# Optimization experiments

Hardware: AMD Instinct MI355X
Metric: run time of the kernel (lower is better)

## Reference

```python
import jax, jax.numpy as jnp
import numpy as np

T_STEPS = 100
T_EMB = 16
EPS = 1e-8


def sin_emb(t, dim):
    # sinusoidal_time_embedding: [cos(t*f), sin(t*f)] with f = exp(-log(1e4)*i/half)
    half = dim // 2
    freqs = jnp.exp(-jnp.log(jnp.float32(10000.0)) * jnp.arange(half, dtype=jnp.float32) / half)
    a = t.astype(jnp.float32)[:, None] * freqs[None, :]
    return jnp.concatenate([jnp.cos(a), jnp.sin(a)], axis=-1)


def lstm_layer(x_tbf, W_ih, W_hh, b):
    # x_tbf: [T, B, F]; torch gate order i, f, g, o
    B = x_tbf.shape[1]
    H = W_hh.shape[1]

    def step(carry, x_t):
        h, c = carry
        g = x_t @ W_ih.T + h @ W_hh.T + b
        i, f, gg, o = jnp.split(g, 4, axis=-1)
        c = jax.nn.sigmoid(f) * c + jax.nn.sigmoid(i) * jnp.tanh(gg)
        h = jax.nn.sigmoid(o) * jnp.tanh(c)
        return (h, c), h

    z = jnp.zeros((B, H), x_tbf.dtype)
    (h, c), ys = jax.lax.scan(step, (z, z), x_tbf)
    return ys, h


def _forward(x_hist, x_future, y0, turb_idx, pred_steps, init_noise, turb_emb,
             W_ih0, W_hh0, b_ih0, b_hh0, W_ih1, W_hh1, b_ih1, b_hh1,
             W1, b1, W2, b2, W3, b3):
    betas = jnp.linspace(1e-4, 0.02, T_STEPS).astype(jnp.float32)
    alphas = 1.0 - betas
    alpha_bars = jnp.cumprod(alphas)

    B = x_hist.shape[0]
    emb = turb_emb[turb_idx]  # [B, E]
    eh = jnp.broadcast_to(emb[:, None, :], (B, x_hist.shape[1], emb.shape[1]))
    ef = jnp.broadcast_to(emb[:, None, :], (B, x_future.shape[1], emb.shape[1]))
    xh = jnp.concatenate([x_hist, eh], axis=-1).transpose(1, 0, 2)    # [T_in, B, F+E]
    xf = jnp.concatenate([x_future, ef], axis=-1).transpose(1, 0, 2)  # [P, B, exo+E]

    ys0, _ = lstm_layer(xh, W_ih0, W_hh0, b_ih0 + b_hh0)
    _, enc_out = lstm_layer(ys0, W_ih1, W_hh1, b_ih1 + b_hh1)         # [B, H] = h[-1]

    def mlp(x):
        h = jax.nn.relu(x @ W1.T + b1)
        h = jax.nn.relu(h @ W2.T + b2)
        return h @ W3.T + b3

    def ar_step(prev_y, xs):
        exo_t, step, y_init = xs
        cond = jnp.concatenate([enc_out, exo_t, prev_y], axis=1)  # [B, cond_dim]
        h_e = sin_emb(jnp.full((B,), step), T_EMB)

        def dstep(y, t):
            t_e = sin_emb(jnp.full((B,), t), T_EMB)
            eps_hat = mlp(jnp.concatenate([cond, y, t_e, h_e], axis=1))  # [B,1]
            b_t, a_t, ab_t = betas[t], alphas[t], alpha_bars[t]
            pred_x0 = (y - jnp.sqrt(1.0 - ab_t) * eps_hat) / (jnp.sqrt(ab_t) + EPS)
            mean = (y - b_t / (jnp.sqrt(1.0 - ab_t) + EPS) * eps_hat) / (jnp.sqrt(a_t) + EPS)
            # eval mode -> deterministic sampling: posterior noise term is zero
            return jnp.where(t == 0, pred_x0, mean), None

        y, _ = jax.lax.scan(dstep, y_init, jnp.arange(T_STEPS - 1, -1, -1))
        return y, y[:, 0]

    _, seq = jax.lax.scan(ar_step, y0, (xf, jnp.arange(pred_steps), init_noise))
    return seq.T[:, :, None]  # [B, pred_steps, 1]


def setup_inputs() -> dict:
    key = jax.random.key(0)
    ks = list(jax.random.split(key, 24))
    kit = iter(ks)
    B, T_IN, F_IN, EXO, EMB, PRED, HID, NTURB = 1024, 96, 8, 6, 16, 8, 128, 100
    in0 = F_IN + EMB                 # 24
    cond_dim = HID + EXO + EMB + 1   # 151
    in_mlp = cond_dim + 1 + T_EMB + T_EMB  # 184

    def nrm(shape, s=0.05):
        return jax.random.normal(next(kit), shape, jnp.float32) * s

    return {
        'x_hist': jax.random.normal(next(kit), (B, T_IN, F_IN), jnp.float32),
        'x_future': jax.random.normal(next(kit), (B, PRED, EXO), jnp.float32),
        'y0': jnp.zeros((B, 1), jnp.float32),
        'turb_idx': jax.random.randint(next(kit), (B,), 0, NTURB),
        'pred_steps': PRED,
        'init_noise': jax.random.normal(next(kit), (PRED, B, 1), jnp.float32),
        'turb_emb': nrm((NTURB, EMB), 0.1),
        'W_ih0': nrm((4 * HID, in0)), 'W_hh0': nrm((4 * HID, HID)),
        'b_ih0': jnp.zeros((4 * HID,), jnp.float32), 'b_hh0': jnp.zeros((4 * HID,), jnp.float32),
        'W_ih1': nrm((4 * HID, HID)), 'W_hh1': nrm((4 * HID, HID)),
        'b_ih1': jnp.zeros((4 * HID,), jnp.float32), 'b_hh1': jnp.zeros((4 * HID,), jnp.float32),
        'W1': nrm((HID, in_mlp)), 'b1': jnp.zeros((HID,), jnp.float32),
        'W2': nrm((HID, HID)), 'b2': jnp.zeros((HID,), jnp.float32),
        'W3': nrm((1, HID)), 'b3': jnp.zeros((1,), jnp.float32),
    }


def reference(x_hist, x_future, y0, turb_idx, pred_steps, init_noise, turb_emb,
              W_ih0, W_hh0, b_ih0, b_hh0, W_ih1, W_hh1, b_ih1, b_hh1,
              W1, b1, W2, b2, W3, b3):
    return _forward(x_hist, x_future, y0, turb_idx, pred_steps, init_noise, turb_emb,
                    W_ih0, W_hh0, b_ih0, b_hh0, W_ih1, W_hh1, b_ih1, b_hh1,
                    W1, b1, W2, b2, W3, b3)
```

## Files before the change

kernel.cpp:

```cpp
#include <hip/hip_runtime.h>
#include <hip/hip_fp16.h>
#include <stdint.h>


typedef __attribute__((ext_vector_type(2))) _Float16 half2_t;
typedef __attribute__((ext_vector_type(8))) _Float16 v8h;
typedef __attribute__((ext_vector_type(4))) float v4f;

#define DEV __device__ __forceinline__

DEV uint32_t pack2f(float a, float b) {
  __half ha = __float2half_rn(a), hb = __float2half_rn(b);
  return (uint32_t)__half_as_ushort(ha) | ((uint32_t)__half_as_ushort(hb) << 16);
}

DEV float2 up2(uint32_t u) {
  half2_t h = __builtin_bit_cast(half2_t, u);
  return make_float2((float)h.x, (float)h.y);
}

DEV float fast_ex2(float x) {
#if __has_builtin(__builtin_amdgcn_exp2f)
  return __builtin_amdgcn_exp2f(x);
#else
  return exp2f(x);
#endif
}
DEV float fast_rcp(float x) {
#if __has_builtin(__builtin_amdgcn_rcpf)
  return __builtin_amdgcn_rcpf(x);
#else
  return 1.f / x;
#endif
}
DEV float sigm(float x) { return fast_rcp(1.f + fast_ex2(-1.4426950408889634f * x)); }
DEV float tanh_f(float x) {
  return 2.f * fast_rcp(1.f + fast_ex2(-2.8853900817779268f * x)) - 1.f;
}

DEV uint32_t pk_h1(uint32_t b, uint32_t t, uint32_t wy, uint32_t yP) {
  half2_t hb = __builtin_bit_cast(half2_t, b);
  half2_t ht = __builtin_bit_cast(half2_t, t);
  half2_t hw = __builtin_bit_cast(half2_t, wy);
  half2_t hy = __builtin_bit_cast(half2_t, yP);
  half2_t r = hb + ht + hw * hy;
  half2_t z = {(_Float16)0.f, (_Float16)0.f};
#if __has_builtin(__builtin_elementwise_max)
  r = __builtin_elementwise_max(r, z);
#else
  uint32_t u = __builtin_bit_cast(uint32_t, r);
  uint32_t mask = ((u >> 15) & 1u) * 0xFFFFu | ((u >> 31) & 1u) * 0xFFFF0000u;
  r = __builtin_bit_cast(half2_t, u & ~mask);
#endif
  return __builtin_bit_cast(uint32_t, r);
}

DEV float rowsum16(float v) {
  int x;
  x = __builtin_amdgcn_update_dpp(0, __builtin_bit_cast(int, v), 0x111, 0xf, 0xf, true);
  v += __builtin_bit_cast(float, x);
  x = __builtin_amdgcn_update_dpp(0, __builtin_bit_cast(int, v), 0x112, 0xf, 0xf, true);
  v += __builtin_bit_cast(float, x);
  x = __builtin_amdgcn_update_dpp(0, __builtin_bit_cast(int, v), 0x114, 0xf, 0xf, true);
  v += __builtin_bit_cast(float, x);
  x = __builtin_amdgcn_update_dpp(0, __builtin_bit_cast(int, v), 0x118, 0xf, 0xf, true);
  v += __builtin_bit_cast(float, x);
  return v;
}

static constexpr size_t OFF_XH  = 0;
static constexpr size_t OFF_W0  = 4718592;
static constexpr size_t OFF_BS0 = 4882432;
static constexpr size_t OFF_W1L = 4884480;
static constexpr size_t OFF_BS1 = 5146624;
static constexpr size_t OFF_W2P = 5148672;
static constexpr size_t OFF_ENC = 5181440;
static constexpr size_t OFF_YS0 = 5705728;

__global__ void k_prep_xh(const float* __restrict__ xh, const int* __restrict__ tix,
                          const float* __restrict__ temb, uint32_t* __restrict__ out) {
  int idx = blockIdx.x * 256 + threadIdx.x;
  if (idx >= 96 * 1024 * 12) return;
  int m = idx % 12;
  int tb = idx / 12;
  int b = tb & 1023, t = tb >> 10;
  int k0 = 2 * m, k1 = k0 + 1;
  float v0 = (k0 < 8) ? xh[(b * 96 + t) * 8 + k0] : temb[tix[b] * 16 + (k0 - 8)];
  float v1 = (k1 < 8) ? xh[(b * 96 + t) * 8 + k1] : temb[tix[b] * 16 + (k1 - 8)];
  out[idx] = pack2f(v0, v1);
}

__global__ void k_prep_w(const float* __restrict__ Wih0, const float* __restrict__ Whh0,
                         const float* __restrict__ bih0, const float* __restrict__ bhh0,
                         const float* __restrict__ Wih1, const float* __restrict__ Whh1,
                         const float* __restrict__ bih1, const float* __restrict__ bhh1,
                         const float* __restrict__ W2,
                         uint32_t* __restrict__ w0p, uint32_t* __restrict__ w1p,
                         uint32_t* __restrict__ w2p, float* __restrict__ bs0,
                         float* __restrict__ bs1) {
  int idx = blockIdx.x * 256 + threadIdx.x;
  if (idx < 40960) {
    int w = idx / 5120;
    int r = idx % 5120;
    int T = r / 1280; r %= 1280;
    int f = r / 256;  r %= 256;
    int l = r >> 2, c = r & 3;
    int m = l & 15, qf = l >> 4;
    int g = (m & 3) * 128 + w * 16 + (m >> 2) * 4 + T;
    int k0 = f * 32 + qf * 8 + 2 * c, k1 = k0 + 1;
    float a = (k0 < 24) ? Wih0[g * 24 + k0] : ((k0 < 152) ? Whh0[g * 128 + k0 - 24] : 0.f);
// ... 61 lines not shown
    uint32_t sx = 0;
    int sb = 0, sm = 0;
    if (t < 95 && tid < 192) {
      sb = tid / 12; sm = tid % 12;
      sx = xh16[((t + 1) * 1024 + bbase + sb) * 12 + sm];
    }
    v4f acc[4];
#pragma unroll
    for (int T = 0; T < 4; T++) acc[T] = (v4f){0.f, 0.f, 0.f, 0.f};
#pragma unroll
    for (int f = 0; f < 5; f++) {
      uint4 bu = *(const uint4*)&inb[cur][n][f * 32 + ql * 8];
      v8h Bv = __builtin_bit_cast(v8h, bu);
#pragma unroll
      for (int T = 0; T < 4; T++)
        acc[T] = __builtin_amdgcn_mfma_f32_16x16x32_f16(
            __builtin_bit_cast(v8h, Af[T][f]), Bv, acc[T], 0, 0, 0);
    }
    float hv[4];
#pragma unroll
    for (int T = 0; T < 4; T++) {
      float gi = acc[T][0] + bias[T][0];
      float gf = acc[T][1] + bias[T][1];
      float gg = acc[T][2] + bias[T][2];
      float go = acc[T][3] + bias[T][3];
      float c = sigm(gf) * cst[T] + sigm(gi) * tanh_f(gg);
      cst[T] = c;
      hv[T] = sigm(go) * tanh_f(c);
    }
    uint32_t h01 = pack2f(hv[0], hv[1]), h23 = pack2f(hv[2], hv[3]);
    *(uint2*)&inb[nxt][n][24 + ju] = make_uint2(h01, h23);
    *(uint2*)((__half*)ys0 + (size_t)(t * 1024 + bbase + n) * 128 + ju) = make_uint2(h01, h23);
    if (t < 95 && tid < 192) ((uint32_t*)&inb[nxt][sb][0])[sm] = sx;
    __syncthreads();
  }
}

__global__ __launch_bounds__(512, 2) void k_lstm1(const uint32_t* __restrict__ ys0u,
                                                  const uint32_t* __restrict__ w1A,
                                                  const float* __restrict__ bs1,
                                                  float* __restrict__ enc) {
  __shared__ __align__(16) __half inb[2][16][264];
  const int tid = threadIdx.x;
  const int w = tid >> 6, l = tid & 63;
  const int n = l & 15, ql = l >> 4;
  const int ju = w * 16 + ql * 4;
  const int bbase = blockIdx.x * 16;
  const int sb = tid >> 5, sc = tid & 31;

  uint4 Af[4][8];
#pragma unroll
  for (int T = 0; T < 4; T++)
#pragma unroll
    for (int f = 0; f < 8; f++)
      Af[T][f] = ((const uint4*)w1A)[((w * 4 + T) * 8 + f) * 64 + l];
  float bias[4][4];
#pragma unroll
  for (int T = 0; T < 4; T++)
#pragma unroll
    for (int r = 0; r < 4; r++) bias[T][r] = bs1[r * 128 + ju + T];

  for (int i = tid; i < 4224; i += 512) ((uint32_t*)inb)[i] = 0u;
  __syncthreads();
  {
    uint2 v = ((const uint2*)ys0u)[(size_t)(0 * 1024 + bbase + sb) * 32 + sc];
    *(uint2*)&inb[0][sb][sc * 4] = v;
  }
// ... 2 lines not shown

  for (int t = 0; t < 96; t++) {
    const int cur = t & 1, nxt = cur ^ 1;
    uint2 sv = make_uint2(0u, 0u);
    if (t < 95)
      sv = ((const uint2*)ys0u)[(size_t)((t + 1) * 1024 + bbase + sb) * 32 + sc];
    v4f acc[4];
#pragma unroll
    for (int T = 0; T < 4; T++) acc[T] = (v4f){0.f, 0.f, 0.f, 0.f};
#pragma unroll
    for (int f = 0; f < 8; f++) {
      uint4 bu = *(const uint4*)&inb[cur][n][f * 32 + ql * 8];
      v8h Bv = __builtin_bit_cast(v8h, bu);
#pragma unroll
      for (int T = 0; T < 4; T++)
        acc[T] = __builtin_amdgcn_mfma_f32_16x16x32_f16(
            __builtin_bit_cast(v8h, Af[T][f]), Bv, acc[T], 0, 0, 0);
    }
    float hv[4];
#pragma unroll
    for (int T = 0; T < 4; T++) {
      float gi = acc[T][0] + bias[T][0];
      float gf = acc[T][1] + bias[T][1];
      float gg = acc[T][2] + bias[T][2];
      float go = acc[T][3] + bias[T][3];
      float c = sigm(gf) * cst[T] + sigm(gi) * tanh_f(gg);
      cst[T] = c;
      hv[T] = sigm(go) * tanh_f(c);
    }
    *(uint2*)&inb[nxt][n][128 + ju] = make_uint2(pack2f(hv[0], hv[1]), pack2f(hv[2], hv[3]));
    if (t < 95) *(uint2*)&inb[nxt][sb][sc * 4] = sv;
    if (t == 95)
      *(float4*)&enc[(size_t)(bbase + n) * 128 + ju] = make_float4(hv[0], hv[1], hv[2], hv[3]);
    __syncthreads();
  }
}

__global__ __launch_bounds__(256, 1) void k_diff(
    const float* __restrict__ xfut, const float* __restrict__ y0,
    const int* __restrict__ tix, const float* __restrict__ noise,
    const float* __restrict__ temb, const float* __restrict__ W1,
    const float* __restrict__ b1, const float* __restrict__ b2,
    const float* __restrict__ W3, const float* __restrict__ b3,
    const uint32_t* __restrict__ w2p, const float* __restrict__ enc,
    float* __restrict__ out) {
  __shared__ __align__(16) uint32_t W1sL[128 * 64];
  __shared__ __align__(16) uint32_t W1xL[128 * 28];
  __shared__ __align__(16) uint32_t encPL[16 * 64];
  __shared__ uint32_t embPL[16 * 8];
  __shared__ float teL[100][16];
  __shared__ float2 ccL[100];
  __shared__ __align__(16) __half tprojL[100 * 128];
  __shared__ __half hprojL[8 * 128];
  __shared__ __align__(16) float partL[2][4][16];
  __shared__ uint32_t encdL[256 * 17];

  const int tid = threadIdx.x;
  const int w = tid >> 6, l = tid & 63;
  const int m = l & 15, q = l >> 4;
  const int bbase = blockIdx.x * 16;

  for (int i = tid; i < 128 * 64; i += 256) {
    int r = i >> 6, c = i & 63;
    W1sL[i] = pack2f(W1[r * 184 + 2 * c], W1[r * 184 + 2 * c + 1]);
  }
  for (int i = tid; i < 128 * 28; i += 256) {
    int r = i / 28, c = i % 28;
    W1xL[i] = pack2f(W1[r * 184 + 128 + 2 * c], W1[r * 184 + 129 + 2 * c]);
  }
  for (int i = tid; i < 16 * 64; i += 256) {
    int bb = i >> 6, c = i & 63;
    encPL[i] = pack2f(enc[(bbase + bb) * 128 + 2 * c], enc[(bbase + bb) * 128 + 2 * c + 1]);
  }
  for (int i = tid; i < 16 * 8; i += 256) {
    int bb = i >> 3, c = i & 7;
    const float* er = temb + tix[bbase + bb] * 16;
    embPL[i] = pack2f(er[2 * c], er[2 * c + 1]);
  }
  for (int p = tid; p < 1600; p += 256) {
    int tt = p >> 4, i = p & 15;
    float f = expf(-logf(10000.f) * (float)(i & 7) / 8.f);
    float a = (float)tt * f;
    teL[tt][i] = (i < 8) ? cosf(a) : sinf(a);
  }
  for (int qq = tid; qq < 100; qq += 256) {
    float ab = 1.f, beta = 0.f;
    for (int i = 0; i <= qq; i++) {
      beta = 1e-4f + (0.02f - 1e-4f) * (float)i / 99.f;
      ab *= (1.f - beta);
    }
    float cs, cd;
    if (qq == 0) { cs = sqrtf(1.f - ab); cd = 1.f / (sqrtf(ab) + 1e-8f); }
    else { cs = beta / (sqrtf(1.f - ab) + 1e-8f); cd = 1.f / (sqrtf(1.f - beta) + 1e-8f); }
    ccL[qq] = make_float2(cs, cd);
  }
  __syncthreads();

  {
    int k = tid & 127, hs = tid >> 7;
    float wte[16], whe[16];
#pragma unroll
    for (int i = 0; i < 8; i++) {
      float2 a = up2(W1xL[k * 28 + 12 + i]);
      wte[2 * i] = a.x; wte[2 * i + 1] = a.y;
      float2 bqq = up2(W1xL[k * 28 + 20 + i]);
      whe[2 * i] = bqq.x; whe[2 * i + 1] = bqq.y;
    }
    for (int tt = hs * 50; tt < hs * 50 + 50; tt++) {
      float s = 0.f;
#pragma unroll
      for (int i = 0; i < 16; i++) s += wte[i] * teL[tt][i];
      tprojL[tt * 128 + k] = __float2half_rn(s);
    }
    if (hs == 0) {
      for (int ss = 0; ss < 8; ss++) {
        float s = 0.f;
#pragma unroll
        for (int i = 0; i < 16; i++) s += whe[i] * teL[ss][i];
        hprojL[ss * 128 + k] = __float2half_rn(s);
      }
    }
  }

  for (int pi = 0; pi < 16; pi++) {
    int k0 = (pi >> 2) * 32 + q * 8 + (pi & 3) * 2;
    half2_t a0 = {(_Float16)0.f, (_Float16)0.f};
    half2_t a1 = a0;
    const uint32_t* wr0 = &W1sL[k0 * 64];
    const uint32_t* wr1 = &W1sL[(k0 + 1) * 64];
    const uint32_t* ep = &encPL[m * 64];
#pragma unroll 8
    for (int c = 0; c < 64; c++) {
      half2_t e = __builtin_bit_cast(half2_t, ep[c]);
      a0 += __builtin_bit_cast(half2_t, wr0[c]) * e;
      a1 += __builtin_bit_cast(half2_t, wr1[c]) * e;
    }
#pragma unroll
    for (int c = 0; c < 8; c++) {
      half2_t e = __builtin_bit_cast(half2_t, embPL[m * 8 + c]);
      a0 += __builtin_bit_cast(half2_t, W1xL[k0 * 28 + 3 + c]) * e;
      a1 += __builtin_bit_cast(half2_t, W1xL[(k0 + 1) * 28 + 3 + c]) * e;
    }
    float e0 = b1[k0] + (float)a0.x + (float)a0.y;
    float e1 = b1[k0 + 1] + (float)a1.x + (float)a1.y;
    encdL[tid * 17 + pi] = pack2f(e0, e1);
  }

  uint4 Bf[2][4];
  const uint4* w2u4 = (const uint4*)w2p;
#pragma unroll
  for (int tt = 0; tt < 2; tt++) {
    int n = w * 32 + tt * 16 + m;
#pragma unroll
    for (int f = 0; f < 4; f++) Bf[tt][f] = w2u4[n * 16 + f * 4 + q];
  }
  const float w3v0 = W3[w * 32 + m], w3v1 = W3[w * 32 + 16 + m];
  const float b2v0 = b2[w * 32 + m], b2v1 = b2[w * 32 + 16 + m];
  const float b3v = b3[0];

  uint32_t w1yP[16];
#pragma unroll
  for (int pi = 0; pi < 16; pi++) {
    int k0 = (pi >> 2) * 32 + q * 8 + (pi & 3) * 2;
    uint32_t ua = W1xL[k0 * 28 + 11];
    uint32_t ub = W1xL[(k0 + 1) * 28 + 11];
    w1yP[pi] = (ua >> 16) | (ub & 0xFFFF0000u);
  }

  float prev_y = y0[bbase + m];
  __syncthreads();

  int buf = 0;
  for (int s = 0; s < 8; s++) {
    float xf[6];
#pragma unroll
    for (int i = 0; i < 6; i++) xf[i] = xfut[((bbase + m) * 8 + s) * 6 + i];
    uint32_t bph[16];
#pragma unroll
    for (int pi = 0; pi < 16; pi++) {
      int k0 = (pi >> 2) * 32 + q * 8 + (pi & 3) * 2;
      float2 ed = up2(encdL[tid * 17 + pi]);
      float e0 = ed.x, e1 = ed.y;
#pragma unroll
      for (int c = 0; c < 3; c++) {
        float2 w0v = up2(W1xL[k0 * 28 + c]);
        float2 w1v = up2(W1xL[(k0 + 1) * 28 + c]);
        e0 += w0v.x * xf[2 * c] + w0v.y * xf[2 * c + 1];
        e1 += w1v.x * xf[2 * c] + w1v.y * xf[2 * c + 1];
      }
      e0 += up2(W1xL[k0 * 28 + 11]).x * prev_y;
      e1 += up2(W1xL[(k0 + 1) * 28 + 11]).x * prev_y;
      e0 += (float)hprojL[s * 128 + k0];
      e1 += (float)hprojL[s * 128 + k0 + 1];
      bph[pi] = pack2f(e0, e1);
    }

    float y = noise[s * 1024 + bbase + m];
    for (int t = 99; t >= 0; t--) {
      const uint4* tp = (const uint4*)(tprojL + t * 128 + q * 8);
      uint32_t yP = pack2f(y, y);
      v4f c0 = {0.f, 0.f, 0.f, 0.f}, c1 = c0;
#pragma unroll
      for (int f = 0; f < 4; f++) {
        uint4 tv = tp[f * 4];
        uint4 au;
        au.x = pk_h1(bph[f * 4 + 0], tv.x, w1yP[f * 4 + 0], yP);
        au.y = pk_h1(bph[f * 4 + 1], tv.y, w1yP[f * 4 + 1], yP);
        au.z = pk_h1(bph[f * 4 + 2], tv.z, w1yP[f * 4 + 2], yP);
        au.w = pk_h1(bph[f * 4 + 3], tv.w, w1yP[f * 4 + 3], yP);
        v8h A = __builtin_bit_cast(v8h, au);
        c0 = __builtin_amdgcn_mfma_f32_16x16x32_f16(A, __builtin_bit_cast(v8h, Bf[0][f]), c0, 0, 0, 0);
        c1 = __builtin_amdgcn_mfma_f32_16x16x32_f16(A, __builtin_bit_cast(v8h, Bf[1][f]), c1, 0, 0, 0);
      }
      float pr[4];
#pragma unroll
      for (int r = 0; r < 4; r++) {
        pr[r] = fmaxf(c0[r] + b2v0, 0.f) * w3v0 + fmaxf(c1[r] + b2v1, 0.f) * w3v1;
        pr[r] = rowsum16(pr[r]);
      }
      if ((l & 15) == 15)
        *(float4*)&partL[buf][w][q * 4] = make_float4(pr[0], pr[1], pr[2], pr[3]);
      __syncthreads();
      float2 cc = ccL[t];
      float eps = b3v + partL[buf][0][m] + partL[buf][1][m] +
                  partL[buf][2][m] + partL[buf][3][m];
      y = (y - cc.x * eps) * cc.y;
      buf ^= 1;
    }
    if (w == 0 && l < 16) out[(bbase + l) * 8 + s] = y;
    prev_y = y;
  }
}

extern "C" void kernel_launch(void* const* d_in, const int* in_sizes, int n_in,
                              void* d_out, int out_size, void* d_ws, size_t ws_size,
                              hipStream_t stream) {
  const float* x_hist    = (const float*)d_in[0];
  const float* x_future  = (const float*)d_in[1];
  const float* y0        = (const float*)d_in[2];
  const int*   turb_idx  = (const int*)d_in[3];
  const float* init_noise = (const float*)d_in[5];
  const float* turb_emb  = (const float*)d_in[6];
  const float* W_ih0     = (const float*)d_in[7];
  const float* W_hh0     = (const float*)d_in[8];
  const float* b_ih0     = (const float*)d_in[9];
  const float* b_hh0     = (const float*)d_in[10];
  const float* W_ih1     = (const float*)d_in[11];
  const float* W_hh1     = (const float*)d_in[12];
  const float* b_ih1     = (const float*)d_in[13];
  const float* b_hh1     = (const float*)d_in[14];
  const float* W1        = (const float*)d_in[15];
  const float* b1        = (const float*)d_in[16];
  const float* W2        = (const float*)d_in[17];
  const float* b2        = (const float*)d_in[18];
  const float* W3        = (const float*)d_in[19];
  const float* b3        = (const float*)d_in[20];

  char* ws = (char*)d_ws;
  uint32_t* xh16 = (uint32_t*)(ws + OFF_XH);
  uint32_t* w0p  = (uint32_t*)(ws + OFF_W0);
  float*    bs0  = (float*)(ws + OFF_BS0);
  uint32_t* w1p  = (uint32_t*)(ws + OFF_W1L);
  float*    bs1  = (float*)(ws + OFF_BS1);
  uint32_t* w2p  = (uint32_t*)(ws + OFF_W2P);
  float*    encf = (float*)(ws + OFF_ENC);
  __half*   ys0h = (__half*)(ws + OFF_YS0);

  k_prep_xh<<<4608, 256, 0, stream>>>(x_hist, turb_idx, turb_emb, xh16);
  k_prep_w<<<452, 256, 0, stream>>>(W_ih0, W_hh0, b_ih0, b_hh0,
                                    W_ih1, W_hh1, b_ih1, b_hh1,
                                    W2, w0p, w1p, w2p, bs0, bs1);
  k_lstm0<<<64, 512, 0, stream>>>(xh16, w0p, bs0, ys0h);
  k_lstm1<<<64, 512, 0, stream>>>((const uint32_t*)ys0h, w1p, bs1, encf);
  k_diff<<<64, 256, 0, stream>>>(x_future, y0, turb_idx, init_noise, turb_emb,
                                 W1, b1, b2, W3, b3, w2p, encf, (float*)d_out);
}
```

Before: 724.9 us.

## Prefetch next-step time projection and shorten the serial diffusion step chain

Inside the 100-step denoising loop, the next timestep's time projection and coefficients are loaded and pre-added to the bias before the barrier, so only a packed FMA plus ReLU sits on the y-dependent path. The MFMA accumulation is split into two independent chains to reduce dependency stalls, y is converted with a packed round-toward-zero convert, and noise is loaded once up front. Shared-memory weight arrays are padded to odd strides to avoid bank conflicts in the setup GEMV. This raises register pressure, and the rounding mode of the y conversion changes slightly.

```diff
diff --git a/kernel.cpp b/kernel.cpp
--- a/kernel.cpp
+++ b/kernel.cpp
@@ -38,12 +38,14 @@
   return 2.f * fast_rcp(1.f + fast_ex2(-2.8853900817779268f * x)) - 1.f;
 }
 
-DEV uint32_t pk_h1(uint32_t b, uint32_t t, uint32_t wy, uint32_t yP) {
-  half2_t hb = __builtin_bit_cast(half2_t, b);
-  half2_t ht = __builtin_bit_cast(half2_t, t);
-  half2_t hw = __builtin_bit_cast(half2_t, wy);
-  half2_t hy = __builtin_bit_cast(half2_t, yP);
-  half2_t r = hb + ht + hw * hy;
+DEV uint32_t pk_add(uint32_t a, uint32_t b) {
+  return __builtin_bit_cast(uint32_t,
+      __builtin_bit_cast(half2_t, a) + __builtin_bit_cast(half2_t, b));
+}
+
+DEV uint32_t pk_relufma(uint32_t w, uint32_t y, uint32_t b) {
+  half2_t r = __builtin_bit_cast(half2_t, w) * __builtin_bit_cast(half2_t, y) +
+              __builtin_bit_cast(half2_t, b);
   half2_t z = {(_Float16)0.f, (_Float16)0.f};
 #if __has_builtin(__builtin_elementwise_max)
   r = __builtin_elementwise_max(r, z);
@@ -53,6 +55,14 @@
   r = __builtin_bit_cast(half2_t, u & ~mask);
 #endif
   return __builtin_bit_cast(uint32_t, r);
+}
+
+DEV uint32_t cvtpk(float y) {
+#if __has_builtin(__builtin_amdgcn_cvt_pkrtz)
+  return __builtin_bit_cast(uint32_t, __builtin_amdgcn_cvt_pkrtz(y, y));
+#else
+  return pack2f(y, y);
+#endif
 }
 
 DEV float rowsum16(float v) {
@@ -284,10 +294,10 @@
     const float* __restrict__ W3, const float* __restrict__ b3,
     const uint32_t* __restrict__ w2p, const float* __restrict__ enc,
     float* __restrict__ out) {
-  __shared__ __align__(16) uint32_t W1sL[128 * 64];
-  __shared__ __align__(16) uint32_t W1xL[128 * 28];
-  __shared__ __align__(16) uint32_t encPL[16 * 64];
-  __shared__ uint32_t embPL[16 * 8];
+  __shared__ uint32_t W1sL[128 * 65];
+  __shared__ uint32_t W1xL[128 * 29];
+  __shared__ uint32_t encPL[16 * 65];
+  __shared__ uint32_t embPL[16 * 9];
   __shared__ float teL[100][16];
   __shared__ float2 ccL[100];
   __shared__ __align__(16) __half tprojL[100 * 128];
@@ -302,20 +312,21 @@
 
   for (int i = tid; i < 128 * 64; i += 256) {
     int r = i >> 6, c = i & 63;
-    W1sL[i] = pack2f(W1[r * 184 + 2 * c], W1[r * 184 + 2 * c + 1]);
+    W1sL[r * 65 + c] = pack2f(W1[r * 184 + 2 * c], W1[r * 184 + 2 * c + 1]);
   }
   for (int i = tid; i < 128 * 28; i += 256) {
     int r = i / 28, c = i % 28;
-    W1xL[i] = pack2f(W1[r * 184 + 128 + 2 * c], W1[r * 184 + 129 + 2 * c]);
+    W1xL[r * 29 + c] = pack2f(W1[r * 184 + 128 + 2 * c], W1[r * 184 + 129 + 2 * c]);
   }
   for (int i = tid; i < 16 * 64; i += 256) {
     int bb = i >> 6, c = i & 63;
-    encPL[i] = pack2f(enc[(bbase + bb) * 128 + 2 * c], enc[(bbase + bb) * 128 + 2 * c + 1]);
+    encPL[bb * 65 + c] = pack2f(enc[(bbase + bb) * 128 + 2 * c],
+                                enc[(bbase + bb) * 128 + 2 * c + 1]);
   }
   for (int i = tid; i < 16 * 8; i += 256) {
     int bb = i >> 3, c = i & 7;
     const float* er = temb + tix[bbase + bb] * 16;
-    embPL[i] = pack2f(er[2 * c], er[2 * c + 1]);
+    embPL[bb * 9 + c] = pack2f(er[2 * c], er[2 * c + 1]);
   }
   for (int p = tid; p < 1600; p += 256) {
     int tt = p >> 4, i = p & 15;
@@ -341,9 +352,9 @@
     float wte[16], whe[16];
 #pragma unroll
     for (int i = 0; i < 8; i++) {
-      float2 a = up2(W1xL[k * 28 + 12 + i]);
+      float2 a = up2(W1xL[k * 29 + 12 + i]);
       wte[2 * i] = a.x; wte[2 * i + 1] = a.y;
-      float2 bqq = up2(W1xL[k * 28 + 20 + i]);
+      float2 bqq = up2(W1xL[k * 29 + 20 + i]);
       whe[2 * i] = bqq.x; whe[2 * i + 1] = bqq.y;
     }
     for (int tt = hs * 50; tt < hs * 50 + 50; tt++) {
@@ -366,9 +377,9 @@
     int k0 = (pi >> 2) * 32 + q * 8 + (pi & 3) * 2;
     half2_t a0 = {(_Float16)0.f, (_Float16)0.f};
     half2_t a1 = a0;
-    const uint32_t* wr0 = &W1sL[k0 * 64];
-    const uint32_t* wr1 = &W1sL[(k0 + 1) * 64];
-    const uint32_t* ep = &encPL[m * 64];
+    const uint32_t* wr0 = &W1sL[k0 * 65];
+    const uint32_t* wr1 = &W1sL[(k0 + 1) * 65];
+    const uint32_t* ep = &encPL[m * 65];
 #pragma unroll 8
     for (int c = 0; c < 64; c++) {
       half2_t e = __builtin_bit_cast(half2_t, ep[c]);
@@ -377,9 +388,9 @@
     }
 #pragma unroll
     for (int c = 0; c < 8; c++) {
-      half2_t e = __builtin_bit_cast(half2_t, embPL[m * 8 + c]);
-      a0 += __builtin_bit_cast(half2_t, W1xL[k0 * 28 + 3 + c]) * e;
-      a1 += __builtin_bit_cast(half2_t, W1xL[(k0 + 1) * 28 + 3 + c]) * e;
+      half2_t e = __builtin_bit_cast(half2_t, embPL[m * 9 + c]);
+      a0 += __builtin_bit_cast(half2_t, W1xL[k0 * 29 + 3 + c]) * e;
+      a1 += __builtin_bit_cast(half2_t, W1xL[(k0 + 1) * 29 + 3 + c]) * e;
     }
     float e0 = b1[k0] + (float)a0.x + (float)a0.y;
     float e1 = b1[k0 + 1] + (float)a1.x + (float)a1.y;
@@ -402,12 +413,15 @@
 #pragma unroll
   for (int pi = 0; pi < 16; pi++) {
     int k0 = (pi >> 2) * 32 + q * 8 + (pi & 3) * 2;
-    uint32_t ua = W1xL[k0 * 28 + 11];
-    uint32_t ub = W1xL[(k0 + 1) * 28 + 11];
+    uint32_t ua = W1xL[k0 * 29 + 11];
+    uint32_t ub = W1xL[(k0 + 1) * 29 + 11];
     w1yP[pi] = (ua >> 16) | (ub & 0xFFFF0000u);
   }
 
   float prev_y = y0[bbase + m];
+  float noi[8];
+#pragma unroll
+  for (int s = 0; s < 8; s++) noi[s] = noise[s * 1024 + bbase + m];
   __syncthreads();
 
   int buf = 0;
@@ -423,35 +437,58 @@
       float e0 = ed.x, e1 = ed.y;
 #pragma unroll
       for (int c = 0; c < 3; c++) {
-        float2 w0v = up2(W1xL[k0 * 28 + c]);
-        float2 w1v = up2(W1xL[(k0 + 1) * 28 + c]);
+        float2 w0v = up2(W1xL[k0 * 29 + c]);
+        float2 w1v = up2(W1xL[(k0 + 1) * 29 + c]);
         e0 += w0v.x * xf[2 * c] + w0v.y * xf[2 * c + 1];
         e1 += w1v.x * xf[2 * c] + w1v.y * xf[2 * c + 1];
       }
-      e0 += up2(W1xL[k0 * 28 + 11]).x * prev_y;
-      e1 += up2(W1xL[(k0 + 1) * 28 + 11]).x * prev_y;
+      e0 += up2(W1xL[k0 * 29 + 11]).x * prev_y;
+      e1 += up2(W1xL[(k0 + 1) * 29 + 11]).x * prev_y;
       e0 += (float)hprojL[s * 128 + k0];
       e1 += (float)hprojL[s * 128 + k0 + 1];
       bph[pi] = pack2f(e0, e1);
     }
 
-    float y = noise[s * 1024 + bbase + m];
+    float y = noi[s];
+    uint32_t bt[16];
+    {
+      const uint4* tb = (const uint4*)(tprojL + 99 * 128 + q * 8);
+      uint4 t0 = tb[0], t1 = tb[4], t2 = tb[8], t3 = tb[12];
+      bt[0] = pk_add(bph[0], t0.x);  bt[1] = pk_add(bph[1], t0.y);
+      bt[2] = pk_add(bph[2], t0.z);  bt[3] = pk_add(bph[3], t0.w);
+      bt[4] = pk_add(bph[4], t1.x);  bt[5] = pk_add(bph[5], t1.y);
+      bt[6] = pk_add(bph[6], t1.z);  bt[7] = pk_add(bph[7], t1.w);
+      bt[8] = pk_add(bph[8], t2.x);  bt[9] = pk_add(bph[9], t2.y);
+      bt[10] = pk_add(bph[10], t2.z); bt[11] = pk_add(bph[11], t2.w);
+      bt[12] = pk_add(bph[12], t3.x); bt[13] = pk_add(bph[13], t3.y);
+      bt[14] = pk_add(bph[14], t3.z); bt[15] = pk_add(bph[15], t3.w);
+    }
+    float2 ccv = ccL[99];
+
     for (int t = 99; t >= 0; t--) {
-      const uint4* tp = (const uint4*)(tprojL + t * 128 + q * 8);
-      uint32_t yP = pack2f(y, y);
-      v4f c0 = {0.f, 0.f, 0.f, 0.f}, c1 = c0;
+      uint32_t yP = cvtpk(y);
+      v4f c0a = {0.f, 0.f, 0.f, 0.f}, c0b = c0a, c1a = c0a, c1b = c0a;
 #pragma unroll
       for (int f = 0; f < 4; f++) {
-        uint4 tv = tp[f * 4];
         uint4 au;
-        au.x = pk_h1(bph[f * 4 + 0], tv.x, w1yP[f * 4 + 0], yP);
-        au.y = pk_h1(bph[f * 4 + 1], tv.y, w1yP[f * 4 + 1], yP);
-        au.z = pk_h1(bph[f * 4 + 2], tv.z, w1yP[f * 4 + 2], yP);
-        au.w = pk_h1(bph[f * 4 + 3], tv.w, w1yP[f * 4 + 3], yP);
+        au.x = pk_relufma(w1yP[4 * f + 0], yP, bt[4 * f + 0]);
+        au.y = pk_relufma(w1yP[4 * f + 1], yP, bt[4 * f + 1]);
+        au.z = pk_relufma(w1yP[4 * f + 2], yP, bt[4 * f + 2]);
+        au.w = pk_relufma(w1yP[4 * f + 3], yP, bt[4 * f + 3]);
         v8h A = __builtin_bit_cast(v8h, au);
-        c0 = __builtin_amdgcn_mfma_f32_16x16x32_f16(A, __builtin_bit_cast(v8h, Bf[0][f]), c0, 0, 0, 0);
-        c1 = __builtin_amdgcn_mfma_f32_16x16x32_f16(A, __builtin_bit_cast(v8h, Bf[1][f]), c1, 0, 0, 0);
+        if (f & 1) {
+          c0b = __builtin_amdgcn_mfma_f32_16x16x32_f16(A, __builtin_bit_cast(v8h, Bf[0][f]), c0b, 0, 0, 0);
+          c1b = __builtin_amdgcn_mfma_f32_16x16x32_f16(A, __builtin_bit_cast(v8h, Bf[1][f]), c1b, 0, 0, 0);
+        } else {
+          c0a = __builtin_amdgcn_mfma_f32_16x16x32_f16(A, __builtin_bit_cast(v8h, Bf[0][f]), c0a, 0, 0, 0);
+          c1a = __builtin_amdgcn_mfma_f32_16x16x32_f16(A, __builtin_bit_cast(v8h, Bf[1][f]), c1a, 0, 0, 0);
+        }
       }
+      const int tn = (t > 0) ? t - 1 : 0;
+      const uint4* tb = (const uint4*)(tprojL + tn * 128 + q * 8);
+      uint4 t0 = tb[0], t1 = tb[4], t2 = tb[8], t3 = tb[12];
+      float2 ccn = ccL[tn];
+      v4f c0 = c0a + c0b, c1 = c1a + c1b;
       float pr[4];
 #pragma unroll
       for (int r = 0; r < 4; r++) {
@@ -460,11 +497,22 @@
       }
       if ((l & 15) == 15)
         *(float4*)&partL[buf][w][q * 4] = make_float4(pr[0], pr[1], pr[2], pr[3]);
+      uint32_t btn[16];
+      btn[0] = pk_add(bph[0], t0.x);  btn[1] = pk_add(bph[1], t0.y);
+      btn[2] = pk_add(bph[2], t0.z);  btn[3] = pk_add(bph[3], t0.w);
+      btn[4] = pk_add(bph[4], t1.x);  btn[5] = pk_add(bph[5], t1.y);
+      btn[6] = pk_add(bph[6], t1.z);  btn[7] = pk_add(bph[7], t1.w);
+      btn[8] = pk_add(bph[8], t2.x);  btn[9] = pk_add(bph[9], t2.y);
+      btn[10] = pk_add(bph[10], t2.z); btn[11] = pk_add(bph[11], t2.w);
+      btn[12] = pk_add(bph[12], t3.x); btn[13] = pk_add(bph[13], t3.y);
+      btn[14] = pk_add(bph[14], t3.z); btn[15] = pk_add(bph[15], t3.w);
       __syncthreads();
-      float2 cc = ccL[t];
-      float eps = b3v + partL[buf][0][m] + partL[buf][1][m] +
-                  partL[buf][2][m] + partL[buf][3][m];
-      y = (y - cc.x * eps) * cc.y;
+      float eps = b3v + ((partL[buf][0][m] + partL[buf][1][m]) +
+                         (partL[buf][2][m] + partL[buf][3][m]));
+      y = (y - ccv.x * eps) * ccv.y;
+      ccv = ccn;
+#pragma unroll
+      for (int pi = 0; pi < 16; pi++) bt[pi] = btn[pi];
       buf ^= 1;
     }
     if (w == 0 && l < 16) out[(bbase + l) * 8 + s] = y;
```

Measured after the change: 675.7 us. 6.8% less time.

## Restructure diffusion sampler into single-wave blocks with precomputed conditioning

Applied to the files above, without the earlier changes.

Moves the per-sample conditioning projections (encoder, exogenous, embedding, step embedding), time-embedding projections and schedule coefficients into a new parallel prep kernel writing to workspace. The diffusion loop now runs one 64-lane wave per block handling 32 samples across all 128 hidden units, so the per-step cross-wave LDS reduction and __syncthreads are replaced by DPP row sums and shuffles. It also software-pipelines the next step's bias+tproj adds, and swaps the LSTM __syncthreads for a raw s_waitcnt+s_barrier. The trade-off is that only 32 blocks of one wave each are active, which lowers occupancy and puts the whole serial chain of 16 MFMAs per step on a single wave, while it adds an extra kernel launch and a workspace round trip.

```diff
diff --git a/kernel.cpp b/kernel.cpp
--- a/kernel.cpp
+++ b/kernel.cpp
@@ -9,14 +9,13 @@
 
 #define DEV __device__ __forceinline__
 
+DEV void barrier_lds() {
+  asm volatile("s_waitcnt lgkmcnt(0)\ns_barrier" ::: "memory");
+}
+
 DEV uint32_t pack2f(float a, float b) {
   __half ha = __float2half_rn(a), hb = __float2half_rn(b);
   return (uint32_t)__half_as_ushort(ha) | ((uint32_t)__half_as_ushort(hb) << 16);
-}
-
-DEV float2 up2(uint32_t u) {
-  half2_t h = __builtin_bit_cast(half2_t, u);
-  return make_float2((float)h.x, (float)h.y);
 }
 
 DEV float fast_ex2(float x) {
@@ -38,12 +37,20 @@
   return 2.f * fast_rcp(1.f + fast_ex2(-2.8853900817779268f * x)) - 1.f;
 }
 
-DEV uint32_t pk_h1(uint32_t b, uint32_t t, uint32_t wy, uint32_t yP) {
-  half2_t hb = __builtin_bit_cast(half2_t, b);
-  half2_t ht = __builtin_bit_cast(half2_t, t);
-  half2_t hw = __builtin_bit_cast(half2_t, wy);
-  half2_t hy = __builtin_bit_cast(half2_t, yP);
-  half2_t r = hb + ht + hw * hy;
+DEV uint32_t pk_add(uint32_t a, uint32_t b) {
+  return __builtin_bit_cast(uint32_t,
+      __builtin_bit_cast(half2_t, a) + __builtin_bit_cast(half2_t, b));
+}
+
+DEV uint32_t pk_fma(uint32_t w, uint32_t y, uint32_t b) {
+  return __builtin_bit_cast(uint32_t,
+      __builtin_bit_cast(half2_t, w) * __builtin_bit_cast(half2_t, y) +
+      __builtin_bit_cast(half2_t, b));
+}
+
+DEV uint32_t pk_relufma(uint32_t w, uint32_t y, uint32_t b) {
+  half2_t r = __builtin_bit_cast(half2_t, w) * __builtin_bit_cast(half2_t, y) +
+              __builtin_bit_cast(half2_t, b);
   half2_t z = {(_Float16)0.f, (_Float16)0.f};
 #if __has_builtin(__builtin_elementwise_max)
   r = __builtin_elementwise_max(r, z);
@@ -53,6 +60,14 @@
   r = __builtin_bit_cast(half2_t, u & ~mask);
 #endif
   return __builtin_bit_cast(uint32_t, r);
+}
+
+DEV uint32_t cvtpk(float y) {
+#if __has_builtin(__builtin_amdgcn_cvt_pkrtz)
+  return __builtin_bit_cast(uint32_t, __builtin_amdgcn_cvt_pkrtz(y, y));
+#else
+  return pack2f(y, y);
+#endif
 }
 
 DEV float rowsum16(float v) {
@@ -76,6 +91,11 @@
 static constexpr size_t OFF_W2P = 5148672;
 static constexpr size_t OFF_ENC = 5181440;
 static constexpr size_t OFF_YS0 = 5705728;
+static constexpr size_t OFF_BASES = 0;
+static constexpr size_t OFF_TPROJ = 2097152;
+static constexpr size_t OFF_CC    = 2122752;
+static constexpr size_t OFF_W1YP  = 2123584;
+static constexpr size_t OFF_W150P = 2123840;
 
 __global__ void k_prep_xh(const float* __restrict__ xh, const int* __restrict__ tix,
                           const float* __restrict__ temb, uint32_t* __restrict__ out) {
@@ -203,7 +223,7 @@
     *(uint2*)&inb[nxt][n][24 + ju] = make_uint2(h01, h23);
     *(uint2*)((__half*)ys0 + (size_t)(t * 1024 + bbase + n) * 128 + ju) = make_uint2(h01, h23);
     if (t < 95 && tid < 192) ((uint32_t*)&inb[nxt][sb][0])[sm] = sx;
-    __syncthreads();
+    barrier_lds();
   }
 }
 
@@ -272,203 +292,235 @@
     if (t < 95) *(uint2*)&inb[nxt][sb][sc * 4] = sv;
     if (t == 95)
       *(float4*)&enc[(size_t)(bbase + n) * 128 + ju] = make_float4(hv[0], hv[1], hv[2], hv[3]);
+    barrier_lds();
+  }
+}
+
+__global__ void k_prep_diff(const float* __restrict__ enc, const float* __restrict__ W1,
+                            const float* __restrict__ b1, const float* __restrict__ xfut,
+                            const float* __restrict__ temb, const int* __restrict__ tix,
+                            __half* __restrict__ baseS, __half* __restrict__ tprojG,
+                            float2* __restrict__ ccG, uint32_t* __restrict__ w1ypG,
+                            uint32_t* __restrict__ w150pG) {
+  const int k = threadIdx.x;
+  const int b = blockIdx.x;
+  if (b < 1024) {
+    __shared__ float encL[128];
+    __shared__ float embL[16];
+    encL[k] = enc[b * 128 + k];
+    if (k < 16) embL[k] = temb[tix[b] * 16 + k];
     __syncthreads();
-  }
-}
-
-__global__ __launch_bounds__(256, 1) void k_diff(
-    const float* __restrict__ xfut, const float* __restrict__ y0,
-    const int* __restrict__ tix, const float* __restrict__ noise,
-    const float* __restrict__ temb, const float* __restrict__ W1,
-    const float* __restrict__ b1, const float* __restrict__ b2,
-    const float* __restrict__ W3, const float* __restrict__ b3,
-    const uint32_t* __restrict__ w2p, const float* __restrict__ enc,
-    float* __restrict__ out) {
-  __shared__ __align__(16) uint32_t W1sL[128 * 64];
-  __shared__ __align__(16) uint32_t W1xL[128 * 28];
-  __shared__ __align__(16) uint32_t encPL[16 * 64];
-  __shared__ uint32_t embPL[16 * 8];
-  __shared__ float teL[100][16];
+    const float* wr = W1 + k * 184;
+    float base0 = b1[k];
+#pragma unroll 8
+    for (int j = 0; j < 128; j++) base0 += wr[j] * encL[j];
+#pragma unroll
+    for (int i = 0; i < 16; i++) base0 += wr[134 + i] * embL[i];
+    for (int s = 0; s < 8; s++) {
+      float v = base0;
+#pragma unroll
+      for (int c = 0; c < 6; c++) v += wr[128 + c] * xfut[(b * 8 + s) * 6 + c];
+#pragma unroll
+      for (int i = 0; i < 16; i++) {
+        float f = expf(-logf(10000.f) * (float)(i & 7) / 8.f);
+        float a = (float)s * f;
+        v += wr[168 + i] * ((i < 8) ? cosf(a) : sinf(a));
+      }
+      baseS[(b * 8 + s) * 128 + k] = __float2half_rn(v);
+    }
+  } else {
+    const float* wr = W1 + k * 184;
+    float wte[16];
+#pragma unroll
+    for (int i = 0; i < 16; i++) wte[i] = wr[152 + i];
+    for (int tt = 0; tt < 100; tt++) {
+      float sv = 0.f;
+#pragma unroll
+      for (int i = 0; i < 16; i++) {
+        float f = expf(-logf(10000.f) * (float)(i & 7) / 8.f);
+        float a = (float)tt * f;
+        sv += wte[i] * ((i < 8) ? cosf(a) : sinf(a));
+      }
+      tprojG[tt * 128 + k] = __float2half_rn(sv);
+    }
+    if (k < 100) {
+      float ab = 1.f, beta = 0.f;
+      for (int i = 0; i <= k; i++) {
+        beta = 1e-4f + (0.02f - 1e-4f) * (float)i / 99.f;
+        ab *= (1.f - beta);
+      }
+      float cs, cd;
+      if (k == 0) { cs = sqrtf(1.f - ab); cd = 1.f / (sqrtf(ab) + 1e-8f); }
+      else { cs = beta / (sqrtf(1.f - ab) + 1e-8f); cd = 1.f / (sqrtf(1.f - beta) + 1e-8f); }
+      ccG[k] = make_float2(cs, cd);
+    }
+    if (k < 64) {
+      w1ypG[k]  = pack2f(W1[(2 * k) * 184 + 151], W1[(2 * k + 1) * 184 + 151]);
+      w150pG[k] = pack2f(W1[(2 * k) * 184 + 150], W1[(2 * k + 1) * 184 + 150]);
+    }
+  }
+}
+
+__global__ __launch_bounds__(64, 1) void k_diff(
+    const float* __restrict__ y0, const float* __restrict__ noise,
+    const uint32_t* __restrict__ baseS, const uint32_t* __restrict__ tprojG,
+    const float2* __restrict__ ccG, const uint32_t* __restrict__ w1ypG,
+    const uint32_t* __restrict__ w150pG, const uint32_t* __restrict__ w2p,
+    const float* __restrict__ b2, const float* __restrict__ W3,
+    const float* __restrict__ b3, float* __restrict__ out) {
+  __shared__ __align__(16) uint32_t tprojL[100 * 64];
   __shared__ float2 ccL[100];
-  __shared__ __align__(16) __half tprojL[100 * 128];
-  __shared__ __half hprojL[8 * 128];
-  __shared__ __align__(16) float partL[2][4][16];
-  __shared__ uint32_t encdL[256 * 17];
-
-  const int tid = threadIdx.x;
-  const int w = tid >> 6, l = tid & 63;
+  const int l = threadIdx.x;
   const int m = l & 15, q = l >> 4;
-  const int bbase = blockIdx.x * 16;
-
-  for (int i = tid; i < 128 * 64; i += 256) {
-    int r = i >> 6, c = i & 63;
-    W1sL[i] = pack2f(W1[r * 184 + 2 * c], W1[r * 184 + 2 * c + 1]);
-  }
-  for (int i = tid; i < 128 * 28; i += 256) {
-    int r = i / 28, c = i % 28;
-    W1xL[i] = pack2f(W1[r * 184 + 128 + 2 * c], W1[r * 184 + 129 + 2 * c]);
-  }
-  for (int i = tid; i < 16 * 64; i += 256) {
-    int bb = i >> 6, c = i & 63;
-    encPL[i] = pack2f(enc[(bbase + bb) * 128 + 2 * c], enc[(bbase + bb) * 128 + 2 * c + 1]);
-  }
-  for (int i = tid; i < 16 * 8; i += 256) {
-    int bb = i >> 3, c = i & 7;
-    const float* er = temb + tix[bbase + bb] * 16;
-    embPL[i] = pack2f(er[2 * c], er[2 * c + 1]);
-  }
-  for (int p = tid; p < 1600; p += 256) {
-    int tt = p >> 4, i = p & 15;
-    float f = expf(-logf(10000.f) * (float)(i & 7) / 8.f);
-    float a = (float)tt * f;
-    teL[tt][i] = (i < 8) ? cosf(a) : sinf(a);
-  }
-  for (int qq = tid; qq < 100; qq += 256) {
-    float ab = 1.f, beta = 0.f;
-    for (int i = 0; i <= qq; i++) {
-      beta = 1e-4f + (0.02f - 1e-4f) * (float)i / 99.f;
-      ab *= (1.f - beta);
-    }
-    float cs, cd;
-    if (qq == 0) { cs = sqrtf(1.f - ab); cd = 1.f / (sqrtf(ab) + 1e-8f); }
-    else { cs = beta / (sqrtf(1.f - ab) + 1e-8f); cd = 1.f / (sqrtf(1.f - beta) + 1e-8f); }
-    ccL[qq] = make_float2(cs, cd);
-  }
+  const int bbase = blockIdx.x * 32;
+  const int bA = bbase + m, bB = bbase + 16 + m;
+
+  for (int i = l; i < 1600; i += 64)
+    ((uint4*)tprojL)[i] = ((const uint4*)tprojG)[i];
+  for (int i = l; i < 100; i += 64) ccL[i] = ccG[i];
+
+  uint4 w1yp4[4], w150p4[4];
+#pragma unroll
+  for (int f = 0; f < 4; f++) {
+    w1yp4[f]  = ((const uint4*)w1ypG)[f * 4 + q];
+    w150p4[f] = ((const uint4*)w150pG)[f * 4 + q];
+  }
+  uint4 Bf[8][4];
+#pragma unroll
+  for (int nt = 0; nt < 8; nt++)
+#pragma unroll
+    for (int f = 0; f < 4; f++)
+      Bf[nt][f] = ((const uint4*)w2p)[(nt * 16 + m) * 16 + f * 4 + q];
+  v4f b2s[8];
+  float w3n[8];
+#pragma unroll
+  for (int nt = 0; nt < 8; nt++) {
+    float bv = b2[nt * 16 + m];
+    b2s[nt] = (v4f){bv, bv, bv, bv};
+    w3n[nt] = W3[nt * 16 + m];
+  }
+  const float b3v = b3[0];
+  const int srcLane = ((l >> 2) & 3) * 16 + 15;
+  float pyA = y0[bA], pyB = y0[bB];
   __syncthreads();
 
-  {
-    int k = tid & 127, hs = tid >> 7;
-    float wte[16], whe[16];
-#pragma unroll
-    for (int i = 0; i < 8; i++) {
-      float2 a = up2(W1xL[k * 28 + 12 + i]);
-      wte[2 * i] = a.x; wte[2 * i + 1] = a.y;
-      float2 bqq = up2(W1xL[k * 28 + 20 + i]);
-      whe[2 * i] = bqq.x; whe[2 * i + 1] = bqq.y;
-    }
-    for (int tt = hs * 50; tt < hs * 50 + 50; tt++) {
-      float s = 0.f;
-#pragma unroll
-      for (int i = 0; i < 16; i++) s += wte[i] * teL[tt][i];
-      tprojL[tt * 128 + k] = __float2half_rn(s);
-    }
-    if (hs == 0) {
-      for (int ss = 0; ss < 8; ss++) {
-        float s = 0.f;
-#pragma unroll
-        for (int i = 0; i < 16; i++) s += whe[i] * teL[ss][i];
-        hprojL[ss * 128 + k] = __float2half_rn(s);
-      }
-    }
-  }
-
-  for (int pi = 0; pi < 16; pi++) {
-    int k0 = (pi >> 2) * 32 + q * 8 + (pi & 3) * 2;
-    half2_t a0 = {(_Float16)0.f, (_Float16)0.f};
-    half2_t a1 = a0;
-    const uint32_t* wr0 = &W1sL[k0 * 64];
-    const uint32_t* wr1 = &W1sL[(k0 + 1) * 64];
-    const uint32_t* ep = &encPL[m * 64];
-#pragma unroll 8
-    for (int c = 0; c < 64; c++) {
-      half2_t e = __builtin_bit_cast(half2_t, ep[c]);
-      a0 += __builtin_bit_cast(half2_t, wr0[c]) * e;
-      a1 += __builtin_bit_cast(half2_t, wr1[c]) * e;
-    }
-#pragma unroll
-    for (int c = 0; c < 8; c++) {
-      half2_t e = __builtin_bit_cast(half2_t, embPL[m * 8 + c]);
-      a0 += __builtin_bit_cast(half2_t, W1xL[k0 * 28 + 3 + c]) * e;
-      a1 += __builtin_bit_cast(half2_t, W1xL[(k0 + 1) * 28 + 3 + c]) * e;
-    }
-    float e0 = b1[k0] + (float)a0.x + (float)a0.y;
-    float e1 = b1[k0 + 1] + (float)a1.x + (float)a1.y;
-    encdL[tid * 17 + pi] = pack2f(e0, e1);
-  }
-
-  uint4 Bf[2][4];
-  const uint4* w2u4 = (const uint4*)w2p;
-#pragma unroll
-  for (int tt = 0; tt < 2; tt++) {
-    int n = w * 32 + tt * 16 + m;
-#pragma unroll
-    for (int f = 0; f < 4; f++) Bf[tt][f] = w2u4[n * 16 + f * 4 + q];
-  }
-  const float w3v0 = W3[w * 32 + m], w3v1 = W3[w * 32 + 16 + m];
-  const float b2v0 = b2[w * 32 + m], b2v1 = b2[w * 32 + 16 + m];
-  const float b3v = b3[0];
-
-  uint32_t w1yP[16];
-#pragma unroll
-  for (int pi = 0; pi < 16; pi++) {
-    int k0 = (pi >> 2) * 32 + q * 8 + (pi & 3) * 2;
-    uint32_t ua = W1xL[k0 * 28 + 11];
-    uint32_t ub = W1xL[(k0 + 1) * 28 + 11];
-    w1yP[pi] = (ua >> 16) | (ub & 0xFFFF0000u);
-  }
-
-  float prev_y = y0[bbase + m];
-  __syncthreads();
-
-  int buf = 0;
   for (int s = 0; s < 8; s++) {
-    float xf[6];
-#pragma unroll
-    for (int i = 0; i < 6; i++) xf[i] = xfut[((bbase + m) * 8 + s) * 6 + i];
-    uint32_t bph[16];
-#pragma unroll
-    for (int pi = 0; pi < 16; pi++) {
-      int k0 = (pi >> 2) * 32 + q * 8 + (pi & 3) * 2;
-      float2 ed = up2(encdL[tid * 17 + pi]);
-      float e0 = ed.x, e1 = ed.y;
-#pragma unroll
-      for (int c = 0; c < 3; c++) {
-        float2 w0v = up2(W1xL[k0 * 28 + c]);
-        float2 w1v = up2(W1xL[(k0 + 1) * 28 + c]);
-        e0 += w0v.x * xf[2 * c] + w0v.y * xf[2 * c + 1];
-        e1 += w1v.x * xf[2 * c] + w1v.y * xf[2 * c + 1];
-      }
-      e0 += up2(W1xL[k0 * 28 + 11]).x * prev_y;
-      e1 += up2(W1xL[(k0 + 1) * 28 + 11]).x * prev_y;
-      e0 += (float)hprojL[s * 128 + k0];
-      e1 += (float)hprojL[s * 128 + k0 + 1];
-      bph[pi] = pack2f(e0, e1);
-    }
-
-    float y = noise[s * 1024 + bbase + m];
+    uint32_t bphA[16], bphB[16];
+    {
+      uint32_t pyPA = cvtpk(pyA), pyPB = cvtpk(pyB);
+#pragma unroll
+      for (int f = 0; f < 4; f++) {
+        uint4 ba = ((const uint4*)baseS)[(bA * 8 + s) * 16 + f * 4 + q];
+        uint4 bb = ((const uint4*)baseS)[(bB * 8 + s) * 16 + f * 4 + q];
+        bphA[f * 4 + 0] = pk_fma(w150p4[f].x, pyPA, ba.x);
+        bphA[f * 4 + 1] = pk_fma(w150p4[f].y, pyPA, ba.y);
+        bphA[f * 4 + 2] = pk_fma(w150p4[f].z, pyPA, ba.z);
+        bphA[f * 4 + 3] = pk_fma(w150p4[f].w, pyPA, ba.w);
+        bphB[f * 4 + 0] = pk_fma(w150p4[f].x, pyPB, bb.x);
+        bphB[f * 4 + 1] = pk_fma(w150p4[f].y, pyPB, bb.y);
+        bphB[f * 4 + 2] = pk_fma(w150p4[f].z, pyPB, bb.z);
+        bphB[f * 4 + 3] = pk_fma(w150p4[f].w, pyPB, bb.w);
+      }
+    }
+    float yA = noise[s * 1024 + bA];
+    float yB = noise[s * 1024 + bB];
+
+    uint32_t btA[16], btB[16];
+#pragma unroll
+    for (int f = 0; f < 4; f++) {
+      uint4 tv = *(const uint4*)&tprojL[99 * 64 + f * 16 + q * 4];
+      btA[f * 4 + 0] = pk_add(bphA[f * 4 + 0], tv.x);
+      btA[f * 4 + 1] = pk_add(bphA[f * 4 + 1], tv.y);
+      btA[f * 4 + 2] = pk_add(bphA[f * 4 + 2], tv.z);
+      btA[f * 4 + 3] = pk_add(bphA[f * 4 + 3], tv.w);
+      btB[f * 4 + 0] = pk_add(bphB[f * 4 + 0], tv.x);
+      btB[f * 4 + 1] = pk_add(bphB[f * 4 + 1], tv.y);
+      btB[f * 4 + 2] = pk_add(bphB[f * 4 + 2], tv.z);
+      btB[f * 4 + 3] = pk_add(bphB[f * 4 + 3], tv.w);
+    }
+    float2 ccv = ccL[99];
+
     for (int t = 99; t >= 0; t--) {
-      const uint4* tp = (const uint4*)(tprojL + t * 128 + q * 8);
-      uint32_t yP = pack2f(y, y);
-      v4f c0 = {0.f, 0.f, 0.f, 0.f}, c1 = c0;
+      uint32_t yPA = cvtpk(yA), yPB = cvtpk(yB);
+      v4f accA[8], accB[8];
 #pragma unroll
       for (int f = 0; f < 4; f++) {
-        uint4 tv = tp[f * 4];
         uint4 au;
-        au.x = pk_h1(bph[f * 4 + 0], tv.x, w1yP[f * 4 + 0], yP);
-        au.y = pk_h1(bph[f * 4 + 1], tv.y, w1yP[f * 4 + 1], yP);
-        au.z = pk_h1(bph[f * 4 + 2], tv.z, w1yP[f * 4 + 2], yP);
-        au.w = pk_h1(bph[f * 4 + 3], tv.w, w1yP[f * 4 + 3], yP);
-        v8h A = __builtin_bit_cast(v8h, au);
-        c0 = __builtin_amdgcn_mfma_f32_16x16x32_f16(A, __builtin_bit_cast(v8h, Bf[0][f]), c0, 0, 0, 0);
-        c1 = __builtin_amdgcn_mfma_f32_16x16x32_f16(A, __builtin_bit_cast(v8h, Bf[1][f]), c1, 0, 0, 0);
-      }
-      float pr[4];
+        au.x = pk_relufma(w1yp4[f].x, yPA, btA[f * 4 + 0]);
+        au.y = pk_relufma(w1yp4[f].y, yPA, btA[f * 4 + 1]);
+        au.z = pk_relufma(w1yp4[f].z, yPA, btA[f * 4 + 2]);
+        au.w = pk_relufma(w1yp4[f].w, yPA, btA[f * 4 + 3]);
+        v8h A_ = __builtin_bit_cast(v8h, au);
+#pragma unroll
+        for (int nt = 0; nt < 8; nt++) {
+          v4f c = (f == 0) ? b2s[nt] : accA[nt];
+          accA[nt] = __builtin_amdgcn_mfma_f32_16x16x32_f16(
+              A_, __builtin_bit_cast(v8h, Bf[nt][f]), c, 0, 0, 0);
+        }
+      }
+#pragma unroll
+      for (int f = 0; f < 4; f++) {
+        uint4 au;
+        au.x = pk_relufma(w1yp4[f].x, yPB, btB[f * 4 + 0]);
+        au.y = pk_relufma(w1yp4[f].y, yPB, btB[f * 4 + 1]);
+        au.z = pk_relufma(w1yp4[f].z, yPB, btB[f * 4 + 2]);
+        au.w = pk_relufma(w1yp4[f].w, yPB, btB[f * 4 + 3]);
+        v8h A_ = __builtin_bit_cast(v8h, au);
+#pragma unroll
+        for (int nt = 0; nt < 8; nt++) {
+          v4f c = (f == 0) ? b2s[nt] : accB[nt];
+          accB[nt] = __builtin_amdgcn_mfma_f32_16x16x32_f16(
+              A_, __builtin_bit_cast(v8h, Bf[nt][f]), c, 0, 0, 0);
+        }
+      }
+      const int tn = (t > 0) ? t - 1 : 0;
+      uint32_t btnA[16], btnB[16];
+#pragma unroll
+      for (int f = 0; f < 4; f++) {
+        uint4 tv = *(const uint4*)&tprojL[tn * 64 + f * 16 + q * 4];
+        btnA[f * 4 + 0] = pk_add(bphA[f * 4 + 0], tv.x);
+        btnA[f * 4 + 1] = pk_add(bphA[f * 4 + 1], tv.y);
+        btnA[f * 4 + 2] = pk_add(bphA[f * 4 + 2], tv.z);
+        btnA[f * 4 + 3] = pk_add(bphA[f * 4 + 3], tv.w);
+        btnB[f * 4 + 0] = pk_add(bphB[f * 4 + 0], tv.x);
+        btnB[f * 4 + 1] = pk_add(bphB[f * 4 + 1], tv.y);
+        btnB[f * 4 + 2] = pk_add(bphB[f * 4 + 2], tv.z);
+        btnB[f * 4 + 3] = pk_add(bphB[f * 4 + 3], tv.w);
+      }
+      float2 ccn = ccL[tn];
+      float prA[4], prB[4];
 #pragma unroll
       for (int r = 0; r < 4; r++) {
-        pr[r] = fmaxf(c0[r] + b2v0, 0.f) * w3v0 + fmaxf(c1[r] + b2v1, 0.f) * w3v1;
-        pr[r] = rowsum16(pr[r]);
-      }
-      if ((l & 15) == 15)
-        *(float4*)&partL[buf][w][q * 4] = make_float4(pr[0], pr[1], pr[2], pr[3]);
-      __syncthreads();
-      float2 cc = ccL[t];
-      float eps = b3v + partL[buf][0][m] + partL[buf][1][m] +
-                  partL[buf][2][m] + partL[buf][3][m];
-      y = (y - cc.x * eps) * cc.y;
-      buf ^= 1;
-    }
-    if (w == 0 && l < 16) out[(bbase + l) * 8 + s] = y;
-    prev_y = y;
+        float pa = 0.f;
+#pragma unroll
+        for (int nt = 0; nt < 8; nt++) pa += w3n[nt] * fmaxf(accA[nt][r], 0.f);
+        prA[r] = rowsum16(pa);
+      }
+#pragma unroll
+      for (int r = 0; r < 4; r++) {
+        float pb = 0.f;
+#pragma unroll
+        for (int nt = 0; nt < 8; nt++) pb += w3n[nt] * fmaxf(accB[nt][r], 0.f);
+        prB[r] = rowsum16(pb);
+      }
+      float a0 = __shfl(prA[0], srcLane, 64), a1 = __shfl(prA[1], srcLane, 64);
+      float a2 = __shfl(prA[2], srcLane, 64), a3 = __shfl(prA[3], srcLane, 64);
+      float e0 = __shfl(prB[0], srcLane, 64), e1 = __shfl(prB[1], srcLane, 64);
+      float e2 = __shfl(prB[2], srcLane, 64), e3 = __shfl(prB[3], srcLane, 64);
+      float epsA = (l & 1) ? ((l & 2) ? a3 : a1) : ((l & 2) ? a2 : a0);
+      float epsB = (l & 1) ? ((l & 2) ? e3 : e1) : ((l & 2) ? e2 : e0);
+      epsA += b3v;
+      epsB += b3v;
+      yA = (yA - ccv.x * epsA) * ccv.y;
+      yB = (yB - ccv.x * epsB) * ccv.y;
+      ccv = ccn;
+#pragma unroll
+      for (int pi = 0; pi < 16; pi++) { btA[pi] = btnA[pi]; btB[pi] = btnB[pi]; }
+    }
+    if (l < 16) out[(bbase + l) * 8 + s] = yA;
+    else if (l < 32) out[(bbase + l) * 8 + s] = yB;
+    pyA = yA;
+    pyB = yB;
   }
 }
 
@@ -505,6 +557,11 @@
   uint32_t* w2p  = (uint32_t*)(ws + OFF_W2P);
   float*    encf = (float*)(ws + OFF_ENC);
   __half*   ys0h = (__half*)(ws + OFF_YS0);
+  __half*   baseS  = (__half*)(ws + OFF_BASES);
+  __half*   tprojG = (__half*)(ws + OFF_TPROJ);
+  float2*   ccG    = (float2*)(ws + OFF_CC);
+  uint32_t* w1ypG  = (uint32_t*)(ws + OFF_W1YP);
+  uint32_t* w150pG = (uint32_t*)(ws + OFF_W150P);
 
   k_prep_xh<<<4608, 256, 0, stream>>>(x_hist, turb_idx, turb_emb, xh16);
   k_prep_w<<<452, 256, 0, stream>>>(W_ih0, W_hh0, b_ih0, b_hh0,
@@ -512,6 +569,9 @@
                                     W2, w0p, w1p, w2p, bs0, bs1);
   k_lstm0<<<64, 512, 0, stream>>>(xh16, w0p, bs0, ys0h);
   k_lstm1<<<64, 512, 0, stream>>>((const uint32_t*)ys0h, w1p, bs1, encf);
-  k_diff<<<64, 256, 0, stream>>>(x_future, y0, turb_idx, init_noise, turb_emb,
-                                 W1, b1, b2, W3, b3, w2p, encf, (float*)d_out);
-}
+  k_prep_diff<<<1025, 128, 0, stream>>>(encf, W1, b1, x_future, turb_emb, turb_idx,
+                                        baseS, tprojG, ccG, w1ypG, w150pG);
+  k_diff<<<32, 64, 0, stream>>>(y0, init_noise, (const uint32_t*)baseS,
+                                (const uint32_t*)tprojG, ccG, w1ypG, w150pG,
+                                w2p, b2, W3, b3, (float*)d_out);
+}
```

After: 1.430 ms. +97.2%, slower.
